# Optimization experiments

Measured on AMD Instinct MI355X. Metric: run time of the kernel, lower is better.

The kernel has to match this reference:

```python
import jax, jax.numpy as jnp
import numpy as np

B, L, H, NH = 2, 2048, 1024, 16
HD = H // NH  # head dim = 64


def setup_inputs() -> dict:
    key = jax.random.key(0)
    ks = jax.random.split(key, 8)
    s = 0.02  # small init scale for weights
    return {
        "q": jax.random.normal(ks[0], (B, L, H), jnp.float32),
        "k": jax.random.normal(ks[1], (B, L, H), jnp.float32),
        "v": jax.random.normal(ks[2], (B, L, H), jnp.float32),
        "attention_mask": jnp.zeros((B, NH, L, L), jnp.float32),
        "Wq": jax.random.normal(ks[3], (H, H), jnp.float32) * s,
        "bq": jnp.zeros((H,), jnp.float32),
        "Wk": jax.random.normal(ks[4], (H, H), jnp.float32) * s,
        "bk": jnp.zeros((H,), jnp.float32),
        "Wv": jax.random.normal(ks[5], (H, H), jnp.float32) * s,
        "bv": jnp.zeros((H,), jnp.float32),
        "Wo": jax.random.normal(ks[6], (H, H), jnp.float32) * s,
        "bo": jnp.zeros((H,), jnp.float32),
    }


def reference(q, k, v, attention_mask, Wq, bq, Wk, bk, Wv, bv, Wo, bo):
    # Conv1D (GPT-2 style) projections: x @ W + b
    query = q @ Wq + bq  # [B, L, H]
    key = k @ Wk + bk
    value = v @ Wv + bv
    # split heads -> [B, NH, L, HD]
    qh = query.reshape(B, L, NH, HD).transpose(0, 2, 1, 3)
    kh = key.reshape(B, L, NH, HD).transpose(0, 2, 1, 3)
    vh = value.reshape(B, L, NH, HD).transpose(0, 2, 1, 3)
    # scores: [B, NH, L, L]
    w = jnp.einsum("bhqd,bhkd->bhqk", qh, kh) / jnp.sqrt(jnp.float32(HD))
    w = w + attention_mask
    w = jax.nn.softmax(w, axis=-1)  # dropout p=0 -> identity
    out = jnp.einsum("bhqk,bhkd->bhqd", w, vh)  # [B, NH, L, HD]
    # merge heads -> [B, L, H]
    out = out.transpose(0, 2, 1, 3).reshape(B, L, H)
    return out @ Wo + bo
```

## Files before the change

kernel.cpp:

```cpp
#include <hip/hip_runtime.h>

#define NBATCH 2
#define LSEQ   2048
#define NH     16
#define HD     64
#define HDIM   1024
#define MTOK   4096

typedef unsigned short u16;
typedef __attribute__((ext_vector_type(8))) short bf16x8;
typedef __attribute__((ext_vector_type(4))) float f32x4;

__device__ __forceinline__ u16 f2bf(float f) {
  union { float f; unsigned int u; } x; x.f = f;
  return (u16)((x.u + 0x7fffu + ((x.u >> 16) & 1u)) >> 16);
}

__device__ __forceinline__ void gload_lds16(const void* g, void* l) {
  __builtin_amdgcn_global_load_lds(
      (const __attribute__((address_space(1))) unsigned int*)g,
      (__attribute__((address_space(3))) unsigned int*)l, 16, 0, 0);
}

__global__ void cvt3_kernel(const float* __restrict__ q, const float* __restrict__ k,
                            const float* __restrict__ v, u16* __restrict__ xq,
                            u16* __restrict__ xk, u16* __restrict__ xv) {
  const float* in;
  u16* out;
  if (blockIdx.z == 0)      { in = q; out = xq; }
  else if (blockIdx.z == 1) { in = k; out = xk; }
  else                      { in = v; out = xv; }
  int i = blockIdx.x * blockDim.x + threadIdx.x;
  float4 t = ((const float4*)in)[i];
  ushort4 o;
  o.x = f2bf(t.x); o.y = f2bf(t.y); o.z = f2bf(t.z); o.w = f2bf(t.w);
  ((ushort4*)out)[i] = o;
}

__global__ void wt4_kernel(const float* __restrict__ W0, const float* __restrict__ W1,
                           const float* __restrict__ W2, const float* __restrict__ W3,
                           u16* __restrict__ T0, u16* __restrict__ T1,
                           u16* __restrict__ T2, u16* __restrict__ T3) {
  const float* W;
  u16* Wt;
  if (blockIdx.z == 0)      { W = W0; Wt = T0; }
  else if (blockIdx.z == 1) { W = W1; Wt = T1; }
  else if (blockIdx.z == 2) { W = W2; Wt = T2; }
  else                      { W = W3; Wt = T3; }
  __shared__ float tile[64][65];
  const int k0 = (blockIdx.x & 15) << 6;
  const int n0 = (blockIdx.x >> 4) << 6;
  const int t = threadIdx.x;
#pragma unroll
  for (int i = 0; i < 4; ++i) {
    int idx = t + i * 256;
    int r = idx >> 4, c = (idx & 15) << 2;
    float4 v = *(const float4*)&W[(size_t)(k0 + r) * HDIM + n0 + c];
    tile[r][c] = v.x; tile[r][c + 1] = v.y; tile[r][c + 2] = v.z; tile[r][c + 3] = v.w;
  }
  __syncthreads();
#pragma unroll
  for (int i = 0; i < 4; ++i) {
    int idx = t + i * 256;
    int r = idx >> 4, c = (idx & 15) << 2;
    ushort4 o;
    o.x = f2bf(tile[c][r]);     o.y = f2bf(tile[c + 1][r]);
    o.z = f2bf(tile[c + 2][r]); o.w = f2bf(tile[c + 3][r]);
    *(ushort4*)&Wt[(size_t)(n0 + r) * HDIM + k0 + c] = o;
  }
}

template <int MODE>
__device__ __forceinline__ void gemm_core(u16* As, u16* Bs,
    const u16* __restrict__ A, const u16* __restrict__ Bt,
    const float* __restrict__ bias, void* __restrict__ Cout) {
  const int tid = threadIdx.x;
  const int lane = tid & 63, wid = tid >> 6;
  const int l15 = lane & 15, g = lane >> 4;
  const int m0 = blockIdx.y * 128, n0 = blockIdx.x * 128;
  const int wr = wid >> 1, wc = wid & 1;
  f32x4 acc[4][4];
#pragma unroll
  for (int i = 0; i < 4; ++i)
#pragma unroll
    for (int j = 0; j < 4; ++j) acc[i][j] = (f32x4){0.f, 0.f, 0.f, 0.f};

  for (int t = 0; t < HDIM / 64; ++t) {
    const int k0 = t * 64;
    __syncthreads();
#pragma unroll
    for (int i = 0; i < 4; ++i) {
      const int row = wid * 32 + i * 8 + (lane >> 3);
      const int colb = (lane & 7) * 16;
      gload_lds16((const char*)(A + (size_t)(m0 + row) * HDIM + k0) + colb,
                  (char*)As + (wid * 32 + i * 8) * 128);
      gload_lds16((const char*)(Bt + (size_t)(n0 + row) * HDIM + k0) + colb,
                  (char*)Bs + (wid * 32 + i * 8) * 128);
    }
    __syncthreads();
#pragma unroll
    for (int ks = 0; ks < 2; ++ks) {
      bf16x8 a[4], b[4];
#pragma unroll
      for (int i = 0; i < 4; ++i) {
        const int row = wr * 64 + i * 16 + l15;
        a[i] = *(const bf16x8*)((const char*)As + row * 128 + ks * 64 + g * 16);
      }
#pragma unroll
      for (int j = 0; j < 4; ++j) {
        const int row = wc * 64 + j * 16 + l15;
        b[j] = *(const bf16x8*)((const char*)Bs + row * 128 + ks * 64 + g * 16);
      }
#pragma unroll
      for (int i = 0; i < 4; ++i)
#pragma unroll
        for (int j = 0; j < 4; ++j)
          acc[i][j] = __builtin_amdgcn_mfma_f32_16x16x32_bf16(a[i], b[j], acc[i][j], 0, 0, 0);
    }
  }
#pragma unroll
  for (int i = 0; i < 4; ++i) {
    const int mrow = m0 + wr * 64 + i * 16 + 4 * g;
#pragma unroll
    for (int j = 0; j < 4; ++j) {
      const int ncol = n0 + wc * 64 + j * 16 + l15;
      const float bb = bias[ncol];
      if (MODE == 3) {
        float* o = (float*)Cout;
#pragma unroll
        for (int r = 0; r < 4; ++r)
          o[(size_t)(mrow + r) * HDIM + ncol] = acc[i][j][r] + bb;
      } else if (MODE == 2) {
        const int bidx = mrow >> 11, l0 = mrow & (LSEQ - 1);
        const int h = ncol >> 6, d = ncol & 63;
        ushort4 o4;
        o4.x = f2bf(acc[i][j][0] + bb); o4.y = f2bf(acc[i][j][1] + bb);
        o4.z = f2bf(acc[i][j][2] + bb); o4.w = f2bf(acc[i][j][3] + bb);
        *(ushort4*)&((u16*)Cout)[(((size_t)bidx * NH + h) * HD + d) * LSEQ + l0] = o4;
      } else {
        const int h = ncol >> 6, d = ncol & 63;
        u16* o = (u16*)Cout;
#pragma unroll
        for (int r = 0; r < 4; ++r) {
          const int m = mrow + r;
          const int bidx = m >> 11, l = m & (LSEQ - 1);
          o[(((size_t)bidx * NH + h) * LSEQ + l) * HD + d] = f2bf(acc[i][j][r] + bb);
        }
      }
    }
  }
}

__global__ __launch_bounds__(256, 2) void proj_gemm_kernel(
    const u16* __restrict__ xq, const u16* __restrict__ xk, const u16* __restrict__ xv,
    const u16* __restrict__ WqT, const u16* __restrict__ WkT, const u16* __restrict__ WvT,
    const float* __restrict__ bq, const float* __restrict__ bk, const float* __restrict__ bv,
    u16* __restrict__ Qh, u16* __restrict__ Kh, u16* __restrict__ Vt) {
  __shared__ u16 As[128 * 64];
  __shared__ u16 Bs[128 * 64];
  if (blockIdx.z == 0)      gemm_core<0>(As, Bs, xq, WqT, bq, Qh);
  else if (blockIdx.z == 1) gemm_core<0>(As, Bs, xk, WkT, bk, Kh);
  else                      gemm_core<2>(As, Bs, xv, WvT, bv, Vt);
}

__global__ __launch_bounds__(256, 2) void out_gemm_kernel(
    const u16* __restrict__ A, const u16* __restrict__ WoT,
    const float* __restrict__ bo, float* __restrict__ out) {
  __shared__ u16 As[128 * 64];
  __shared__ u16 Bs[128 * 64];
  gemm_core<3>(As, Bs, A, WoT, bo, out);
}

__global__ __launch_bounds__(256, 4) void attn_kernel(
    const u16* __restrict__ Qh, const u16* __restrict__ Kh,
    const u16* __restrict__ Vt, const float* __restrict__ mask,
    u16* __restrict__ Out ) {
  __shared__ u16 Ks[2][64 * 64];
  __shared__ u16 Vs[2][64 * 64];
  __shared__ u16 Ps[4][16 * 64];
  const int lane = threadIdx.x & 63, w = threadIdx.x >> 6;
  const int l15 = lane & 15, g = lane >> 4;
  const int bh = blockIdx.y;
  const int q0 = blockIdx.x * 64 + w * 16;
  const int NT = LSEQ / 64;

  bf16x8 aq[2];
  {
    const u16* qbase = Qh + ((size_t)bh * LSEQ + q0 + l15) * HD;
    aq[0] = *(const bf16x8*)(qbase + g * 8);
    aq[1] = *(const bf16x8*)(qbase + 32 + g * 8);
  }
  f32x4 o_acc[4];
#pragma unroll
  for (int db = 0; db < 4; ++db) o_acc[db] = (f32x4){0.f, 0.f, 0.f, 0.f};
  float m_run = -1e30f, l_run = 0.f;

  const size_t kbase = (size_t)bh * LSEQ * HD;
  const size_t vbase = (size_t)bh * HD * LSEQ;
  const int srow = w * 16 + (lane >> 3);
  const int scolb = (lane & 7) * 16;

#define STAGE(buf, tt) do {                                                    \
    const int kv0_ = (tt) * 64;                                                \
    _Pragma("unroll")                                                          \
    for (int i_ = 0; i_ < 2; ++i_) {                                           \
      const int row_ = srow + i_ * 8;                                          \
      const int cb_ = scolb ^ ((row_ & 7) << 4);                               \
      gload_lds16((const char*)(Kh + kbase + (size_t)(kv0_ + row_) * HD) + cb_,\
                  (char*)Ks[buf] + (w * 16 + i_ * 8) * 128);                   \
      gload_lds16((const char*)(Vt + vbase + (size_t)row_ * LSEQ + kv0_) + cb_,\
                  (char*)Vs[buf] + (w * 16 + i_ * 8) * 128);                   \
    }                                                                          \
  } while (0)

  const float* mrow = mask + ((size_t)bh * LSEQ + q0 + l15) * LSEQ;
  f32x4 mvA[4], mvB[4];

  STAGE(0, 0);
#pragma unroll
  for (int mb = 0; mb < 4; ++mb) {
    mvA[mb] = *(const f32x4*)(mrow + 0 * 64 + mb * 16 + 4 * g);
    mvB[mb] = *(const f32x4*)(mrow + 1 * 64 + mb * 16 + 4 * g);
  }
  __syncthreads();

  u16* pbase = Ps[w];
  const int srcbase = (lane & 48) | ((lane & 48) >> 2);
  const int pswz = (l15 & 7) << 4;

#define TILE_BODY(t, cur, mv) do {                                            \
    if ((t) + 1 < NT) STAGE((cur) ^ 1, (t) + 1);                              \
               \
    f32x4 s_acc[4];                                                           \
    _Pragma("unroll")                                                         \
    for (int mb = 0; mb < 4; ++mb) s_acc[mb] = (f32x4){0.f, 0.f, 0.f, 0.f};   \
    __builtin_amdgcn_s_setprio(1);                                            \
    _Pragma("unroll")                                                         \
    for (int ks = 0; ks < 2; ++ks) {                                          \
      _Pragma("unroll")                                                       \
      for (int mb = 0; mb < 4; ++mb) {                                        \
        const int row = mb * 16 + l15;                                        \
        bf16x8 bk = *(const bf16x8*)((const char*)Ks[cur] + row * 128 +       \
                                     ((ks * 64 + g * 16) ^ ((row & 7) << 4)));\
        s_acc[mb] = __builtin_amdgcn_mfma_f32_16x16x32_bf16(bk, aq[ks],       \
                                                            s_acc[mb], 0,0,0);\
      }                                                                       \
    }                                                                         \
    __builtin_amdgcn_s_setprio(0);                                            \
                              \
    float p[4][4];                                                            \
    float tmax = -1e30f;                                                      \
    _Pragma("unroll")                                                         \
    for (int mb = 0; mb < 4; ++mb)                                            \
      _Pragma("unroll")                                                       \
      for (int r = 0; r < 4; ++r) {                                           \
        p[mb][r] = s_acc[mb][r] * 0.125f + mv[mb][r];                         \
        tmax = fmaxf(tmax, p[mb][r]);                                         \
      }                                                                       \
    tmax = fmaxf(tmax, __shfl_xor(tmax, 16));                                 \
    tmax = fmaxf(tmax, __shfl_xor(tmax, 32));                                 \
    if (!__all(tmax - m_run <= 8.f)) {                     \
      const float mnew = fmaxf(m_run, tmax);                                  \
      const float cf = __expf(m_run - mnew);                                  \
      m_run = mnew;                                                           \
      l_run *= cf;                                                            \
      float cfr[4];                                                           \
      _Pragma("unroll")                                                       \
      for (int r = 0; r < 4; ++r) cfr[r] = __shfl(cf, srcbase + r);           \
      _Pragma("unroll")                                                       \
      for (int db = 0; db < 4; ++db)                                          \
        _Pragma("unroll")                                                     \
        for (int r = 0; r < 4; ++r) o_acc[db][r] *= cfr[r];                   \
    }                                                                         \
    float psum = 0.f;                                                         \
    _Pragma("unroll")                                                         \
    for (int mb = 0; mb < 4; ++mb)                                            \
      _Pragma("unroll")                                                       \
      for (int r = 0; r < 4; ++r) {                                           \
        p[mb][r] = __expf(p[mb][r] - m_run);                                  \
        psum += p[mb][r];                                                     \
      }                                                                       \
    psum += __shfl_xor(psum, 16);                                             \
    psum += __shfl_xor(psum, 32);                                             \
    l_run += psum;                                                            \
                             \
    _Pragma("unroll")                                                         \
    for (int mb = 0; mb < 4; ++mb) {                                          \
      ushort4 pk;                                                             \
      pk.x = f2bf(p[mb][0]); pk.y = f2bf(p[mb][1]);                           \
      pk.z = f2bf(p[mb][2]); pk.w = f2bf(p[mb][3]);                           \
      *(ushort4*)((char*)pbase + l15 * 128 + ((mb * 32 + 8 * g) ^ pswz)) = pk;\
    }                                                                         \
           \
    __builtin_amdgcn_sched_barrier(0);                                        \
    {                                                                         \
      const int tn = ((t) + 2 < NT) ? (t) + 2 : NT - 1;                       \
      const float* mnext = mrow + tn * 64;                                    \
      _Pragma("unroll")                                                       \
      for (int mb = 0; mb < 4; ++mb)                                          \
        mv[mb] = *(const f32x4*)(mnext + mb * 16 + 4 * g);                    \
    }                                                                         \
                      \
    asm volatile("s_waitcnt lgkmcnt(0)" ::: "memory");                        \
    __builtin_amdgcn_sched_barrier(0);                                        \
                                                                \
    __builtin_amdgcn_s_setprio(1);                                            \
    _Pragma("unroll")                                                         \
    for (int s = 0; s < 2; ++s) {                                             \
      bf16x8 pa = *(const bf16x8*)((const char*)pbase + l15 * 128 +           \
                                   ((s * 64 + 16 * g) ^ pswz));               \
      _Pragma("unroll")                                                       \
      for (int db = 0; db < 4; ++db) {                                        \
        const int row = db * 16 + l15;                                        \
        bf16x8 bv = *(const bf16x8*)((const char*)Vs[cur] + row * 128 +       \
                                     ((s * 64 + 16 * g) ^ ((row & 7) << 4))); \
        o_acc[db] = __builtin_amdgcn_mfma_f32_16x16x32_bf16(pa, bv,           \
                                                            o_acc[db], 0,0,0);\
      }                                                                       \
    }                                                                         \
    __builtin_amdgcn_s_setprio(0);                                            \
         \
    asm volatile("s_waitcnt vmcnt(4)" ::: "memory");                          \
    __builtin_amdgcn_s_barrier();                                             \
    __builtin_amdgcn_sched_barrier(0);                                        \
  } while (0)

  for (int t = 0; t < NT; t += 2) {
    TILE_BODY(t, 0, mvA);
    TILE_BODY(t + 1, 1, mvB);
  }
#undef TILE_BODY
#undef STAGE

  const int b = bh >> 4, h = bh & 15;
  float lr[4];
#pragma unroll
  for (int r = 0; r < 4; ++r) lr[r] = __shfl(l_run, srcbase + r);
#pragma unroll
  for (int r = 0; r < 4; ++r) {
    const float inv = 1.f / lr[r];
    const int qg = q0 + 4 * g + r;
    u16* orow = Out + ((size_t)(b * LSEQ + qg) * NH + h) * HD;
#pragma unroll
    for (int db = 0; db < 4; ++db)
      orow[db * 16 + l15] = f2bf(o_acc[db][r] * inv);
  }
}

extern "C" void kernel_launch(void* const* d_in, const int* in_sizes, int n_in,
                              void* d_out, int out_size, void* d_ws, size_t ws_size,
                              hipStream_t stream) {
  (void)in_sizes; (void)n_in; (void)out_size; (void)ws_size;
  const float* q    = (const float*)d_in[0];
  const float* k    = (const float*)d_in[1];
  const float* v    = (const float*)d_in[2];
  const float* mask = (const float*)d_in[3];
  const float* Wq   = (const float*)d_in[4];
  const float* bq   = (const float*)d_in[5];
  const float* Wk   = (const float*)d_in[6];
  const float* bk   = (const float*)d_in[7];
  const float* Wv   = (const float*)d_in[8];
  const float* bv   = (const float*)d_in[9];
  const float* Wo   = (const float*)d_in[10];
  const float* bo   = (const float*)d_in[11];
  float* out = (float*)d_out;

  char* ws = (char*)d_ws;
  const size_t XB = (size_t)MTOK * HDIM * 2;
  const size_t WB = (size_t)HDIM * HDIM * 2;
  u16* xq   = (u16*)(ws);
  u16* xk   = (u16*)(ws + XB);
  u16* xv   = (u16*)(ws + 2 * XB);
  u16* WqT  = (u16*)(ws + 3 * XB);
  u16* WkT  = (u16*)(ws + 3 * XB + WB);
  u16* WvT  = (u16*)(ws + 3 * XB + 2 * WB);
  u16* WoT  = (u16*)(ws + 3 * XB + 3 * WB);
  u16* Qh   = (u16*)(ws + 3 * XB + 4 * WB);
  u16* Kh   = (u16*)(ws + 4 * XB + 4 * WB);
  u16* Vt   = (u16*)(ws + 5 * XB + 4 * WB);
  u16* aout = (u16*)(ws + 6 * XB + 4 * WB);

  cvt3_kernel<<<dim3((MTOK * HDIM) / 4 / 256, 1, 3), 256, 0, stream>>>(
      q, k, v, xq, xk, xv);
  wt4_kernel<<<dim3(256, 1, 4), 256, 0, stream>>>(
      Wq, Wk, Wv, Wo, WqT, WkT, WvT, WoT);
  proj_gemm_kernel<<<dim3(HDIM / 128, MTOK / 128, 3), 256, 0, stream>>>(
      xq, xk, xv, WqT, WkT, WvT, bq, bk, bv, Qh, Kh, Vt);
  attn_kernel<<<dim3(LSEQ / 64, NBATCH * NH), 256, 0, stream>>>(Qh, Kh, Vt, mask, aout);
  out_gemm_kernel<<<dim3(HDIM / 128, MTOK / 128), 256, 0, stream>>>(aout, WoT, bo, out);
}
```

Measured before the change: 233.4 us.

## Merge prep kernels, remap GEMM blocks across XCDs, raise occupancy bound

Merges the fp32-to-bf16 activation conversion and the weight transpose into a single prep kernel, removing one launch. Both GEMM kernels now use a flat 1D grid with a block-index remap, (h&7)*stride + (h>>3), so that consecutive tiles sharing the same A rows are placed on the same XCD, improving L2 reuse. Launch bounds are raised from 2 to 3 blocks per SIMD group, which may constrain register allocation. The prep grid launches many idle blocks in the z=3 slice that return early.

```diff
diff --git a/kernel.cpp b/kernel.cpp
--- a/kernel.cpp
+++ b/kernel.cpp
@@ -22,41 +22,37 @@
       (__attribute__((address_space(3))) unsigned int*)l, 16, 0, 0);
 }
 
-__global__ void cvt3_kernel(const float* __restrict__ q, const float* __restrict__ k,
-                            const float* __restrict__ v, u16* __restrict__ xq,
-                            u16* __restrict__ xk, u16* __restrict__ xv) {
-  const float* in;
-  u16* out;
-  if (blockIdx.z == 0)      { in = q; out = xq; }
-  else if (blockIdx.z == 1) { in = k; out = xk; }
-  else                      { in = v; out = xv; }
-  int i = blockIdx.x * blockDim.x + threadIdx.x;
-  float4 t = ((const float4*)in)[i];
-  ushort4 o;
-  o.x = f2bf(t.x); o.y = f2bf(t.y); o.z = f2bf(t.z); o.w = f2bf(t.w);
-  ((ushort4*)out)[i] = o;
-}
-
-__global__ void wt4_kernel(const float* __restrict__ W0, const float* __restrict__ W1,
-                           const float* __restrict__ W2, const float* __restrict__ W3,
-                           u16* __restrict__ T0, u16* __restrict__ T1,
-                           u16* __restrict__ T2, u16* __restrict__ T3) {
-  const float* W;
-  u16* Wt;
-  if (blockIdx.z == 0)      { W = W0; Wt = T0; }
-  else if (blockIdx.z == 1) { W = W1; Wt = T1; }
-  else if (blockIdx.z == 2) { W = W2; Wt = T2; }
-  else                      { W = W3; Wt = T3; }
+__global__ void prep_kernel(
+    const float* __restrict__ q, const float* __restrict__ k, const float* __restrict__ v,
+    const float* __restrict__ W0, const float* __restrict__ W1,
+    const float* __restrict__ W2, const float* __restrict__ W3,
+    u16* __restrict__ xq, u16* __restrict__ xk, u16* __restrict__ xv,
+    u16* __restrict__ T0, u16* __restrict__ T1, u16* __restrict__ T2,
+    u16* __restrict__ T3) {
   __shared__ float tile[64][65];
-  const int k0 = (blockIdx.x & 15) << 6;
-  const int n0 = (blockIdx.x >> 4) << 6;
+  if (blockIdx.z < 3) {
+    const float* in = (blockIdx.z == 0) ? q : (blockIdx.z == 1) ? k : v;
+    u16* out = (blockIdx.z == 0) ? xq : (blockIdx.z == 1) ? xk : xv;
+    int i = blockIdx.x * blockDim.x + threadIdx.x;
+    float4 t4 = ((const float4*)in)[i];
+    ushort4 o;
+    o.x = f2bf(t4.x); o.y = f2bf(t4.y); o.z = f2bf(t4.z); o.w = f2bf(t4.w);
+    ((ushort4*)out)[i] = o;
+    return;
+  }
+  if (blockIdx.x >= 1024) return;
+  const int sel = blockIdx.x >> 8, bx = blockIdx.x & 255;
+  const float* W = (sel == 0) ? W0 : (sel == 1) ? W1 : (sel == 2) ? W2 : W3;
+  u16* Wt = (sel == 0) ? T0 : (sel == 1) ? T1 : (sel == 2) ? T2 : T3;
+  const int k0 = (bx & 15) << 6;
+  const int n0 = (bx >> 4) << 6;
   const int t = threadIdx.x;
 #pragma unroll
   for (int i = 0; i < 4; ++i) {
     int idx = t + i * 256;
     int r = idx >> 4, c = (idx & 15) << 2;
-    float4 v = *(const float4*)&W[(size_t)(k0 + r) * HDIM + n0 + c];
-    tile[r][c] = v.x; tile[r][c + 1] = v.y; tile[r][c + 2] = v.z; tile[r][c + 3] = v.w;
+    float4 v4 = *(const float4*)&W[(size_t)(k0 + r) * HDIM + n0 + c];
+    tile[r][c] = v4.x; tile[r][c + 1] = v4.y; tile[r][c + 2] = v4.z; tile[r][c + 3] = v4.w;
   }
   __syncthreads();
 #pragma unroll
@@ -71,13 +67,12 @@
 }
 
 template <int MODE>
-__device__ __forceinline__ void gemm_core(u16* As, u16* Bs,
+__device__ __forceinline__ void gemm_core(u16* As, u16* Bs, int m0, int n0,
     const u16* __restrict__ A, const u16* __restrict__ Bt,
     const float* __restrict__ bias, void* __restrict__ Cout) {
   const int tid = threadIdx.x;
   const int lane = tid & 63, wid = tid >> 6;
   const int l15 = lane & 15, g = lane >> 4;
-  const int m0 = blockIdx.y * 128, n0 = blockIdx.x * 128;
   const int wr = wid >> 1, wc = wid & 1;
   f32x4 acc[4][4];
 #pragma unroll
@@ -151,24 +146,31 @@
   }
 }
 
-__global__ __launch_bounds__(256, 2) void proj_gemm_kernel(
+__global__ __launch_bounds__(256, 3) void proj_gemm_kernel(
     const u16* __restrict__ xq, const u16* __restrict__ xk, const u16* __restrict__ xv,
     const u16* __restrict__ WqT, const u16* __restrict__ WkT, const u16* __restrict__ WvT,
     const float* __restrict__ bq, const float* __restrict__ bk, const float* __restrict__ bv,
     u16* __restrict__ Qh, u16* __restrict__ Kh, u16* __restrict__ Vt) {
   __shared__ u16 As[128 * 64];
   __shared__ u16 Bs[128 * 64];
-  if (blockIdx.z == 0)      gemm_core<0>(As, Bs, xq, WqT, bq, Qh);
-  else if (blockIdx.z == 1) gemm_core<0>(As, Bs, xk, WkT, bk, Kh);
-  else                      gemm_core<2>(As, Bs, xv, WvT, bv, Vt);
-}
-
-__global__ __launch_bounds__(256, 2) void out_gemm_kernel(
+  const int h = blockIdx.x;
+  const int l = (h & 7) * 96 + (h >> 3);
+  const int z = l >> 8, rem = l & 255;
+  const int m0 = (rem >> 3) * 128, n0 = (rem & 7) * 128;
+  if (z == 0)      gemm_core<0>(As, Bs, m0, n0, xq, WqT, bq, Qh);
+  else if (z == 1) gemm_core<0>(As, Bs, m0, n0, xk, WkT, bk, Kh);
+  else             gemm_core<2>(As, Bs, m0, n0, xv, WvT, bv, Vt);
+}
+
+__global__ __launch_bounds__(256, 3) void out_gemm_kernel(
     const u16* __restrict__ A, const u16* __restrict__ WoT,
     const float* __restrict__ bo, float* __restrict__ out) {
   __shared__ u16 As[128 * 64];
   __shared__ u16 Bs[128 * 64];
-  gemm_core<3>(As, Bs, A, WoT, bo, out);
+  const int h = blockIdx.x;
+  const int l = (h & 7) * 32 + (h >> 3);
+  const int m0 = (l >> 3) * 128, n0 = (l & 7) * 128;
+  gemm_core<3>(As, Bs, m0, n0, A, WoT, bo, out);
 }
 
 __global__ __launch_bounds__(256, 4) void attn_kernel(
@@ -380,12 +382,10 @@
   u16* Vt   = (u16*)(ws + 5 * XB + 4 * WB);
   u16* aout = (u16*)(ws + 6 * XB + 4 * WB);
 
-  cvt3_kernel<<<dim3((MTOK * HDIM) / 4 / 256, 1, 3), 256, 0, stream>>>(
-      q, k, v, xq, xk, xv);
-  wt4_kernel<<<dim3(256, 1, 4), 256, 0, stream>>>(
-      Wq, Wk, Wv, Wo, WqT, WkT, WvT, WoT);
-  proj_gemm_kernel<<<dim3(HDIM / 128, MTOK / 128, 3), 256, 0, stream>>>(
+  prep_kernel<<<dim3((MTOK * HDIM) / 4 / 256, 1, 4), 256, 0, stream>>>(
+      q, k, v, Wq, Wk, Wv, Wo, xq, xk, xv, WqT, WkT, WvT, WoT);
+  proj_gemm_kernel<<<768, 256, 0, stream>>>(
       xq, xk, xv, WqT, WkT, WvT, bq, bk, bv, Qh, Kh, Vt);
   attn_kernel<<<dim3(LSEQ / 64, NBATCH * NH), 256, 0, stream>>>(Qh, Kh, Vt, mask, aout);
-  out_gemm_kernel<<<dim3(HDIM / 128, MTOK / 128), 256, 0, stream>>>(aout, WoT, bo, out);
-}
+  out_gemm_kernel<<<256, 256, 0, stream>>>(aout, WoT, bo, out);
+}
```

Result: no change. 228.9 us (-1.9%).
